# Kernel optimization log

Hardware: AMD Instinct MI355X
Metric: run time of the kernel (lower is better)

The kernel has to match this reference:

```python
import jax, jax.numpy as jnp
import numpy as np

MU = 0.9
STEPSIZE = 1.0
EPS = 1e-6

N, H, D, M = 1024, 16, 64, 64


def elu_feature_map(x):
    # elu(x) + 1 (the default feature map of linear attention)
    return jax.nn.elu(x) + 1.0


def setup_inputs() -> dict:
    key = jax.random.key(0)
    k1, k2, k3, k4, k5, k6 = jax.random.split(key, 6)
    return {
        "query": jax.random.normal(k1, (N, H, D), dtype=jnp.float32),
        "key": jax.random.normal(k2, (N, H, D), dtype=jnp.float32),
        "value": jax.random.normal(k3, (N, H, M), dtype=jnp.float32),
        "Si": jax.random.normal(k4, (N, H, D, M), dtype=jnp.float32),
        "Zi": jax.random.uniform(k5, (N, H, D), dtype=jnp.float32),
        "Pi": jax.random.normal(k6, (N, H, D, M), dtype=jnp.float32),
    }


def reference(query, key, value, Si, Zi, Pi):
    Q = elu_feature_map(query)  # (N,H,D)
    K = elu_feature_map(key)    # (N,H,D)

    # momentum-accumulated outer-product state update
    Zi_new = Zi + K
    Pi_new = MU * Pi - STEPSIZE * jnp.einsum('nhd,nhm->nhdm', K, value)
    Si_new = Si - Pi_new

    # query read-out with normalization
    Z = 1.0 / (jnp.einsum('nhd,nhd->nh', Q, Zi_new) + EPS)  # (N,H)
    V = jnp.einsum('nhd,nhdm,nh->nhm', Q, Si_new, Z)         # (N,H,M)
    return V, Si_new, Zi_new, Pi_new
```

## Files before the change

### kernel.cpp

```cpp
#include <hip/hip_runtime.h>
#include <math.h>

#define NPAIR 16384
#define DDIM 64
#define MDIM 64

#define V_OFF   0LL
#define SI_OFF  1048576LL
#define ZI_OFF  68157440LL
#define PI_OFF  69206016LL

typedef float v4f __attribute__((ext_vector_type(4)));

__global__ __launch_bounds__(256) void rma_kernel(
    const float* __restrict__ query,
    const float* __restrict__ key,
    const float* __restrict__ value,
    const float* __restrict__ Si,
    const float* __restrict__ Zi,
    const float* __restrict__ Pi,
    float* __restrict__ out)
{
    const int pair = blockIdx.x;
    const int tid  = threadIdx.x;

    __shared__ float Qs[DDIM];
    __shared__ float Ks[DDIM];
    __shared__ float Vls[MDIM];
    __shared__ float Vred[16][68];
    __shared__ float Zinv;

    const long long vecOff = (long long)pair * DDIM;
    const long long matOff = (long long)pair * (DDIM * MDIM);

    const int tm = (tid & 15) << 2;
    const int td = tid >> 4;

    long long flat[4];
    v4f piu[4], siu[4];
    #pragma unroll
    for (int r = 0; r < 4; ++r) {
        const int d = td + 16 * r;
        flat[r] = matOff + (long long)(d * MDIM + tm);
        piu[r] = __builtin_nontemporal_load((const v4f*)(Pi + flat[r]));
        siu[r] = __builtin_nontemporal_load((const v4f*)(Si + flat[r]));
    }

    if (tid < 64) {
        const int d = tid;
        float q  = query[vecOff + d];
        float k  = key[vecOff + d];
        float zi = Zi[vecOff + d];
        float qe = (q > 0.f) ? (q + 1.f) : expf(q);
        float ke = (k > 0.f) ? (k + 1.f) : expf(k);
        float zn = zi + ke;
        Qs[d]  = qe;
        Ks[d]  = ke;
        Vls[d] = value[vecOff + d];
        __builtin_nontemporal_store(zn, out + ZI_OFF + vecOff + d);
        float p = qe * zn;
        #pragma unroll
        for (int off = 32; off > 0; off >>= 1)
            p += __shfl_down(p, off, 64);
        if (tid == 0) Zinv = 1.f / (p + 1e-6f);
    }
    __syncthreads();

    float acc[4] = {0.f, 0.f, 0.f, 0.f};
    const float v0 = Vls[tm + 0], v1 = Vls[tm + 1], v2 = Vls[tm + 2], v3 = Vls[tm + 3];
    #pragma unroll
    for (int r = 0; r < 4; ++r) {
        const int d = td + 16 * r;
        const float kd = Ks[d];
        const float qd = Qs[d];
        v4f pn, sn;
        pn.x = 0.9f * piu[r].x - kd * v0;  sn.x = siu[r].x - pn.x;  acc[0] += qd * sn.x;
        pn.y = 0.9f * piu[r].y - kd * v1;  sn.y = siu[r].y - pn.y;  acc[1] += qd * sn.y;
        pn.z = 0.9f * piu[r].z - kd * v2;  sn.z = siu[r].z - pn.z;  acc[2] += qd * sn.z;
        pn.w = 0.9f * piu[r].w - kd * v3;  sn.w = siu[r].w - pn.w;  acc[3] += qd * sn.w;
        __builtin_nontemporal_store(pn, (v4f*)(out + PI_OFF + flat[r]));
        __builtin_nontemporal_store(sn, (v4f*)(out + SI_OFF + flat[r]));
    }

    Vred[td][tm + 0] = acc[0];
    Vred[td][tm + 1] = acc[1];
    Vred[td][tm + 2] = acc[2];
    Vred[td][tm + 3] = acc[3];
    __syncthreads();

    if (tid < 64) {
        float s = 0.f;
        #pragma unroll
        for (int t = 0; t < 16; ++t) s += Vred[t][tid];
        out[V_OFF + vecOff + tid] = s * Zinv;
    }
}

extern "C" void kernel_launch(void* const* d_in, const int* in_sizes, int n_in,
                              void* d_out, int out_size, void* d_ws, size_t ws_size,
                              hipStream_t stream)
{
    const float* query = (const float*)d_in[0];
    const float* key   = (const float*)d_in[1];
    const float* value = (const float*)d_in[2];
    const float* Si    = (const float*)d_in[3];
    const float* Zi    = (const float*)d_in[4];
    const float* Pi    = (const float*)d_in[5];
    float* out = (float*)d_out;

    rma_kernel<<<NPAIR, 256, 0, stream>>>(query, key, value, Si, Zi, Pi, out);
}
```

Before: 839.0 us.

## Map one wavefront per head-pair and replace LDS reductions with shuffles

Each 64-lane wavefront now handles a whole (n,h) pair, with four pairs per 256-thread block, instead of one block per pair. Shared memory and __syncthreads are replaced by wave shuffles for broadcasting Q/K/V and for reducing the normalizer and output. Each lane now holds 16 float4 loads of Pi and Si in flight, which raises register pressure and may lower occupancy in this bandwidth-bound kernel.

```diff
diff --git a/kernel.cpp b/kernel.cpp
--- a/kernel.cpp
+++ b/kernel.cpp
@@ -21,78 +21,73 @@
     const float* __restrict__ Pi,
     float* __restrict__ out)
 {
-    const int pair = blockIdx.x;
-    const int tid  = threadIdx.x;
-
-    __shared__ float Qs[DDIM];
-    __shared__ float Ks[DDIM];
-    __shared__ float Vls[MDIM];
-    __shared__ float Vred[16][68];
-    __shared__ float Zinv;
+    const int lane = threadIdx.x & 63;
+    const int wv   = threadIdx.x >> 6;
+    const int pair = (blockIdx.x << 2) | wv;
 
     const long long vecOff = (long long)pair * DDIM;
     const long long matOff = (long long)pair * (DDIM * MDIM);
 
-    const int tm = (tid & 15) << 2;
-    const int td = tid >> 4;
+    const float q  = query[vecOff + lane];
+    const float k  = key[vecOff + lane];
+    const float zi = Zi[vecOff + lane];
+    const float vv = value[vecOff + lane];
 
-    long long flat[4];
-    v4f piu[4], siu[4];
+    const int tm = (lane & 15) << 2;
+    const int td = lane >> 4;
+
+    long long flat[16];
+    v4f piu[16], siu[16];
     #pragma unroll
-    for (int r = 0; r < 4; ++r) {
-        const int d = td + 16 * r;
-        flat[r] = matOff + (long long)(d * MDIM + tm);
-        piu[r] = __builtin_nontemporal_load((const v4f*)(Pi + flat[r]));
-        siu[r] = __builtin_nontemporal_load((const v4f*)(Si + flat[r]));
+    for (int rr = 0; rr < 16; ++rr) {
+        const int d = td + (rr << 2);
+        flat[rr] = matOff + (long long)(d * MDIM + tm);
+        piu[rr] = __builtin_nontemporal_load((const v4f*)(Pi + flat[rr]));
+        siu[rr] = __builtin_nontemporal_load((const v4f*)(Si + flat[rr]));
     }
 
-    if (tid < 64) {
-        const int d = tid;
-        float q  = query[vecOff + d];
-        float k  = key[vecOff + d];
-        float zi = Zi[vecOff + d];
-        float qe = (q > 0.f) ? (q + 1.f) : expf(q);
-        float ke = (k > 0.f) ? (k + 1.f) : expf(k);
-        float zn = zi + ke;
-        Qs[d]  = qe;
-        Ks[d]  = ke;
-        Vls[d] = value[vecOff + d];
-        __builtin_nontemporal_store(zn, out + ZI_OFF + vecOff + d);
-        float p = qe * zn;
-        #pragma unroll
-        for (int off = 32; off > 0; off >>= 1)
-            p += __shfl_down(p, off, 64);
-        if (tid == 0) Zinv = 1.f / (p + 1e-6f);
-    }
-    __syncthreads();
+    const float qe = (q > 0.f) ? (q + 1.f) : expf(q);
+    const float ke = (k > 0.f) ? (k + 1.f) : expf(k);
+    const float zn = zi + ke;
+    __builtin_nontemporal_store(zn, out + ZI_OFF + vecOff + lane);
 
-    float acc[4] = {0.f, 0.f, 0.f, 0.f};
-    const float v0 = Vls[tm + 0], v1 = Vls[tm + 1], v2 = Vls[tm + 2], v3 = Vls[tm + 3];
+    float p = qe * zn;
     #pragma unroll
-    for (int r = 0; r < 4; ++r) {
-        const int d = td + 16 * r;
-        const float kd = Ks[d];
-        const float qd = Qs[d];
+    for (int off = 32; off; off >>= 1) p += __shfl_xor(p, off, 64);
+    const float zinv = 1.f / (p + 1e-6f);
+
+    const float v0 = __shfl(vv, tm + 0, 64);
+    const float v1 = __shfl(vv, tm + 1, 64);
+    const float v2 = __shfl(vv, tm + 2, 64);
+    const float v3 = __shfl(vv, tm + 3, 64);
+
+    float acc0 = 0.f, acc1 = 0.f, acc2 = 0.f, acc3 = 0.f;
+    #pragma unroll
+    for (int rr = 0; rr < 16; ++rr) {
+        const int d = td + (rr << 2);
+        const float kd = __shfl(ke, d, 64);
+        const float qd = __shfl(qe, d, 64);
         v4f pn, sn;
-        pn.x = 0.9f * piu[r].x - kd * v0;  sn.x = siu[r].x - pn.x;  acc[0] += qd * sn.x;
-        pn.y = 0.9f * piu[r].y - kd * v1;  sn.y = siu[r].y - pn.y;  acc[1] += qd * sn.y;
-        pn.z = 0.9f * piu[r].z - kd * v2;  sn.z = siu[r].z - pn.z;  acc[2] += qd * sn.z;
-        pn.w = 0.9f * piu[r].w - kd * v3;  sn.w = siu[r].w - pn.w;  acc[3] += qd * sn.w;
-        __builtin_nontemporal_store(pn, (v4f*)(out + PI_OFF + flat[r]));
-        __builtin_nontemporal_store(sn, (v4f*)(out + SI_OFF + flat[r]));
+        pn.x = 0.9f * piu[rr].x - kd * v0;  sn.x = siu[rr].x - pn.x;  acc0 += qd * sn.x;
+        pn.y = 0.9f * piu[rr].y - kd * v1;  sn.y = siu[rr].y - pn.y;  acc1 += qd * sn.y;
+        pn.z = 0.9f * piu[rr].z - kd * v2;  sn.z = siu[rr].z - pn.z;  acc2 += qd * sn.z;
+        pn.w = 0.9f * piu[rr].w - kd * v3;  sn.w = siu[rr].w - pn.w;  acc3 += qd * sn.w;
+        __builtin_nontemporal_store(pn, (v4f*)(out + PI_OFF + flat[rr]));
+        __builtin_nontemporal_store(sn, (v4f*)(out + SI_OFF + flat[rr]));
     }
 
-    Vred[td][tm + 0] = acc[0];
-    Vred[td][tm + 1] = acc[1];
-    Vred[td][tm + 2] = acc[2];
-    Vred[td][tm + 3] = acc[3];
-    __syncthreads();
+    acc0 += __shfl_xor(acc0, 16, 64);  acc0 += __shfl_xor(acc0, 32, 64);
+    acc1 += __shfl_xor(acc1, 16, 64);  acc1 += __shfl_xor(acc1, 32, 64);
+    acc2 += __shfl_xor(acc2, 16, 64);  acc2 += __shfl_xor(acc2, 32, 64);
+    acc3 += __shfl_xor(acc3, 16, 64);  acc3 += __shfl_xor(acc3, 32, 64);
 
-    if (tid < 64) {
-        float s = 0.f;
-        #pragma unroll
-        for (int t = 0; t < 16; ++t) s += Vred[t][tid];
-        out[V_OFF + vecOff + tid] = s * Zinv;
+    if (td == 0) {
+        v4f vout;
+        vout.x = acc0 * zinv;
+        vout.y = acc1 * zinv;
+        vout.z = acc2 * zinv;
+        vout.w = acc3 * zinv;
+        *(v4f*)(out + V_OFF + vecOff + tm) = vout;
     }
 }
 
@@ -108,5 +103,5 @@
     const float* Pi    = (const float*)d_in[5];
     float* out = (float*)d_out;
 
-    rma_kernel<<<NPAIR, 256, 0, stream>>>(query, key, value, Si, Zi, Pi, out);
+    rma_kernel<<<NPAIR / 4, 256, 0, stream>>>(query, key, value, Si, Zi, Pi, out);
 }
```

Result: no change. 837.8 us (-0.1%).
